# Optimization experiments

Hardware: AMD Instinct MI355X
Metric: run time of the kernel (lower is better)

## Reference

```python
import jax, jax.numpy as jnp
import numpy as np

N = 512          # pedestrians in scene
T = 12           # decode steps
OBS = 8
FEAT = 2
LAT = 32
COND = 64
LSTM_IN = 128
HID = 64         # lstm_hidden_size == context_state_size
CTX = 64
EMB = 32         # Pooling_net spatial embedding dim
MLP_IN = EMB + 2 * CTX   # 160
MLP_MID = 64
BOT = CTX        # bottleneck_dim = h_dim
IN_DEC = COND + LAT + CTX + FEAT  # 162


def setup_inputs() -> dict:
    key = jax.random.key(0)
    ks = jax.random.split(key, 24)
    s = 0.1
    return {
        "last_position": jax.random.normal(ks[0], (N, FEAT), jnp.float32),
        "c": jax.random.normal(ks[1], (N, COND), jnp.float32),
        "z": jax.random.normal(ks[2], (N, LAT), jnp.float32),
        "obs_traj_pos": jax.random.normal(ks[3], (OBS, N, FEAT), jnp.float32),
        "nei_index": jax.random.randint(ks[4], (T, N, N), 0, 2, jnp.int32),
        "nei_num_index": jax.random.randint(ks[5], (N,), 0, N, jnp.int32),
        "h0": jax.random.normal(ks[6], (N, HID), jnp.float32),
        "c0": jax.random.normal(ks[7], (N, HID), jnp.float32),
        "eps": jax.random.normal(ks[8], (T, N, FEAT), jnp.float32),
        "W_in": jax.random.normal(ks[9], (IN_DEC, LSTM_IN), jnp.float32) * s,
        "b_in": jnp.zeros((LSTM_IN,), jnp.float32),
        "W_ih": jax.random.normal(ks[10], (4 * HID, LSTM_IN), jnp.float32) * s,
        "W_hh": jax.random.normal(ks[11], (4 * HID, HID), jnp.float32) * s,
        "b_ih": jnp.zeros((4 * HID,), jnp.float32),
        "b_hh": jnp.zeros((4 * HID,), jnp.float32),
        "W_l2p": jax.random.normal(ks[12], (HID // 2 + CTX, FEAT), jnp.float32) * s,
        "b_l2p": jnp.zeros((FEAT,), jnp.float32),
        "W_sp": jax.random.normal(ks[13], (FEAT, EMB), jnp.float32) * s,
        "b_sp": jnp.zeros((EMB,), jnp.float32),
        "W1": jax.random.normal(ks[14], (MLP_IN, MLP_MID), jnp.float32) * s,
        "b1": jnp.zeros((MLP_MID,), jnp.float32),
        "W2": jax.random.normal(ks[15], (MLP_MID, BOT), jnp.float32) * s,
        "b2": jnp.zeros((BOT,), jnp.float32),
    }


def reference(last_position, c, z, obs_traj_pos, nei_index, nei_num_index,
              h0, c0, eps, W_in, b_in, W_ih, W_hh, b_ih, b_hh,
              W_l2p, b_l2p, W_sp, b_sp, W1, b1, W2, b2):
    sg = jax.lax.stop_gradient
    half = HID // 2
    neg_inf = jnp.float32(-jnp.inf)

    def pooling(mask, lstm_state, pos):
        # mask: [N,N] bool; lstm_state: [N,CTX]; pos: [N,2]
        corr = pos[:, None, :] - pos[None, :, :]           # [N,N,2] pos[i]-pos[j]
        r = corr @ W_sp + b_sp                              # [N,N,EMB]
        hj = jnp.broadcast_to(lstm_state[None, :, :], (N, N, CTX))
        hi = jnp.broadcast_to(lstm_state[:, None, :], (N, N, CTX))
        x = jnp.concatenate([r, hj, hi], axis=-1)           # [N,N,160]
        h1 = jax.nn.relu(x @ W1 + b1)
        h2 = jax.nn.relu(h1 @ W2 + b2)                      # [N,N,BOT]
        Hm = jnp.where(mask[:, :, None], h2, neg_inf)       # scatter of valid rows
        pool = Hm.max(axis=1)                               # max over neighbors j
        return jnp.where(pool == neg_inf, 0.0, pool)

    def lstm_cell(x, h, cs):
        gates = x @ W_ih.T + b_ih + h @ W_hh.T + b_hh
        i, f, g, o = jnp.split(gates, 4, axis=-1)
        c_new = jax.nn.sigmoid(f) * cs + jax.nn.sigmoid(i) * jnp.tanh(g)
        h_new = jax.nn.sigmoid(o) * jnp.tanh(c_new)
        return h_new, c_new

    def step(carry, xs):
        prev_pos, h, cs, ctx, cur_abs = carry
        nei_t, eps_t = xs
        emb = jnp.concatenate([sg(prev_pos), sg(c), sg(z), sg(ctx)], axis=-1)
        x = jax.nn.relu(emb @ W_in + b_in)
        h, cs = lstm_cell(x, h, cs)
        ctx = pooling(nei_t > 0, h, cur_abs)
        mu = jnp.concatenate([h[:, :half], ctx], -1) @ W_l2p + b_l2p
        logvar = jnp.concatenate([h[:, half:], ctx], -1) @ W_l2p + b_l2p
        pos = mu + eps_t * jnp.exp(0.5 * logvar)
        cur_abs = sg(cur_abs + pos)
        return (pos, h, cs, ctx, cur_abs), (pos, mu, logvar)

    ctx0 = jnp.zeros((N, CTX), jnp.float32)
    carry0 = (last_position, h0, c0, ctx0, obs_traj_pos[-1])
    _, (pre_pos, mean, var) = jax.lax.scan(step, carry0, (nei_index, eps))
    return pre_pos, mean, var
```

## Files before the change

### kernel.cpp

```cpp
#include <hip/hip_runtime.h>
#include <math.h>

#define NP 512
#define TT 12

typedef float f32x4 __attribute__((ext_vector_type(4)));
typedef __bf16 bf16x8 __attribute__((ext_vector_type(8)));

#define OFF_CURABS 0
#define OFF_Q      2048
#define OFF_P      67584
#define OFF_H      100352
#define OFF_CS     133120
#define OFF_XCZ    165888
#define OFF_WGB    231424
#define OFF_WCTXB  256000
#define OFF_W1B    260096
#define OFF_WIN01  264192
#define OFF_WC     264448
#define OFF_BASE   264576

__global__ __launch_bounds__(256) void init_k(
    const float* __restrict__ obs, const float* __restrict__ cc,
    const float* __restrict__ zz,
    const float* __restrict__ W_in, const float* __restrict__ W_ih,
    const float* __restrict__ W_hh, const float* __restrict__ W_sp,
    const float* __restrict__ b_sp, const float* __restrict__ W1,
    const float* __restrict__ b1, float* __restrict__ ws) {
  if (blockIdx.x < 128) {
    int id = blockIdx.x * 256 + threadIdx.x;
    if (id < 1024) ws[OFF_CURABS + id] = obs[7 * 1024 + id];
    __bf16* wgb = (__bf16*)(ws + OFF_WGB);
    for (int e = id; e < 49152; e += 32768) {
      int k = e >> 8, g = e & 255;
      float v = (k < 128) ? W_ih[g * 128 + k] : W_hh[g * 64 + (k - 128)];
      wgb[e] = (__bf16)v;
    }
    if (id < 8192) {
      int d = id >> 7, k = id & 127;
      ((__bf16*)(ws + OFF_WCTXB))[id] = (__bf16)W_in[(98 + d) * 128 + k];
    }
    if (id < 8192) {
      int r = id >> 6, m = id & 63;
      ((__bf16*)(ws + OFF_W1B))[id] = (__bf16)W1[(32 + r) * 64 + m];
    }
    if (id < 256) ws[OFF_WIN01 + id] = W_in[(id >> 7) * 128 + (id & 127)];
    if (id < 128) {
      int d = id >> 6, m = id & 63;
      float s = 0.f;
      for (int e = 0; e < 32; ++e) s = fmaf(W_sp[d * 32 + e], W1[e * 64 + m], s);
      ws[OFF_WC + id] = s;
    }
    if (id < 64) {
      float s = b1[id];
      for (int e = 0; e < 32; ++e) s = fmaf(b_sp[e], W1[e * 64 + id], s);
      ws[OFF_BASE + id] = s;
    }
  } else {
    int b = blockIdx.x - 128;
    int k = threadIdx.x;
    if (k < 128) {
      float s = 0.f;
      for (int d = 0; d < 64; ++d) s = fmaf(cc[b * 64 + d], W_in[(2 + d) * 128 + k], s);
      for (int d = 0; d < 32; ++d) s = fmaf(zz[b * 32 + d], W_in[(66 + d) * 128 + k], s);
      ws[OFF_XCZ + b * 128 + k] = s;
    }
  }
}

__global__ __launch_bounds__(256) void step_k(
    const float* __restrict__ lastpos, const int* __restrict__ nei,
    const float* __restrict__ h0, const float* __restrict__ c0,
    const float* __restrict__ obs, const float* __restrict__ epsin,
    const float* __restrict__ b_in,
    const float* __restrict__ b_ih, const float* __restrict__ b_hh,
    const float* __restrict__ Wl2p, const float* __restrict__ bl2p,
    const float* __restrict__ W2, const float* __restrict__ b2,
    float* __restrict__ out, float* __restrict__ ws, int s) {
  __shared__ __align__(16) __bf16 W2T[64 * 72];
  __shared__ int   ml[512];
  __shared__ float wcl[128], basev[64];
  __shared__ float red[4][64];
  __shared__ float hloc[64], csloc[64], ctxloc[64], prevp[2], pxy[2];
  __shared__ float xpart[2][128], xvec[128], gl[256];

  int t = threadIdx.x;
  int b = blockIdx.x;
  int lane = t & 63, w = t >> 6;
  int quad = lane >> 4, col = lane & 15;

  if (t < 64) {
    if (s == 0) { hloc[t] = h0[b * 64 + t]; csloc[t] = c0[b * 64 + t]; ctxloc[t] = 0.f; }
    else        { hloc[t] = ws[OFF_H + b * 64 + t]; csloc[t] = ws[OFF_CS + b * 64 + t]; }
    basev[t] = ws[OFF_BASE + t];
  } else if (t < 192) {
    wcl[t - 64] = ws[OFF_WC + (t - 64)];
  }
  if (s == 0 && t < 2) {
    prevp[t] = lastpos[b * 2 + t];
    pxy[t]   = obs[7 * 1024 + b * 2 + t];
  }
  if (s > 0) {
    for (int e = t; e < 4096; e += 256)
      W2T[(e & 63) * 72 + (e >> 6)] = (__bf16)W2[e];
    const int* neirow = nei + ((size_t)(s - 1) * NP + b) * NP;
    for (int j = t; j < 512; j += 256) ml[j] = neirow[j];
  }
  __syncthreads();

  if (s > 0) {
    int st = s - 1;
    const float* Qb = ws + OFF_Q + (st & 1) * 32768;
    bf16x8 bf00 = *(const bf16x8*)&W2T[(0 * 16 + col) * 72 + 0 * 32 + quad * 8];
    bf16x8 bf01 = *(const bf16x8*)&W2T[(0 * 16 + col) * 72 + 1 * 32 + quad * 8];
    bf16x8 bf10 = *(const bf16x8*)&W2T[(1 * 16 + col) * 72 + 0 * 32 + quad * 8];
    bf16x8 bf11 = *(const bf16x8*)&W2T[(1 * 16 + col) * 72 + 1 * 32 + quad * 8];
    bf16x8 bf20 = *(const bf16x8*)&W2T[(2 * 16 + col) * 72 + 0 * 32 + quad * 8];
    bf16x8 bf21 = *(const bf16x8*)&W2T[(2 * 16 + col) * 72 + 1 * 32 + quad * 8];
    bf16x8 bf30 = *(const bf16x8*)&W2T[(3 * 16 + col) * 72 + 0 * 32 + quad * 8];
    bf16x8 bf31 = *(const bf16x8*)&W2T[(3 * 16 + col) * 72 + 1 * 32 + quad * 8];
    float pl0[8], pl1[8];
    #pragma unroll
    for (int e = 0; e < 8; ++e) {
      pl0[e] = ws[OFF_P + b * 64 + quad * 8 + e];
      pl1[e] = ws[OFF_P + b * 64 + 32 + quad * 8 + e];
    }
    float vmax0 = -1e30f, vmax1 = -1e30f, vmax2 = -1e30f, vmax3 = -1e30f;

    for (int c = 0; c < 8; ++c) {
      int j0 = w * 128 + c * 16;
      int jr = (j0 + col) * 64 + quad * 8;
      f32x4 qa = *(const f32x4*)&Qb[jr];
      f32x4 qb = *(const f32x4*)&Qb[jr + 4];
      f32x4 qc = *(const f32x4*)&Qb[jr + 32];
      f32x4 qd = *(const f32x4*)&Qb[jr + 36];
      bf16x8 a0, a1;
      #pragma unroll
      for (int e = 0; e < 4; ++e) {
        a0[e]     = (__bf16)fmaxf(qa[e] + pl0[e],     0.f);
        a0[e + 4] = (__bf16)fmaxf(qb[e] + pl0[e + 4], 0.f);
        a1[e]     = (__bf16)fmaxf(qc[e] + pl1[e],     0.f);
        a1[e + 4] = (__bf16)fmaxf(qd[e] + pl1[e + 4], 0.f);
      }
      int mrow = j0 + quad * 4;
      bool mk0 = ml[mrow] > 0, mk1 = ml[mrow + 1] > 0,
           mk2 = ml[mrow + 2] > 0, mk3 = ml[mrow + 3] > 0;
      f32x4 acc;
      acc = (f32x4){0.f, 0.f, 0.f, 0.f};
      acc = __builtin_amdgcn_mfma_f32_16x16x32_bf16(a0, bf00, acc, 0, 0, 0);
      acc = __builtin_amdgcn_mfma_f32_16x16x32_bf16(a1, bf01, acc, 0, 0, 0);
      vmax0 = fmaxf(vmax0, mk0 ? acc[0] : -1e30f);
      vmax0 = fmaxf(vmax0, mk1 ? acc[1] : -1e30f);
      vmax0 = fmaxf(vmax0, mk2 ? acc[2] : -1e30f);
      vmax0 = fmaxf(vmax0, mk3 ? acc[3] : -1e30f);
      acc = (f32x4){0.f, 0.f, 0.f, 0.f};
      acc = __builtin_amdgcn_mfma_f32_16x16x32_bf16(a0, bf10, acc, 0, 0, 0);
      acc = __builtin_amdgcn_mfma_f32_16x16x32_bf16(a1, bf11, acc, 0, 0, 0);
      vmax1 = fmaxf(vmax1, mk0 ? acc[0] : -1e30f);
      vmax1 = fmaxf(vmax1, mk1 ? acc[1] : -1e30f);
      vmax1 = fmaxf(vmax1, mk2 ? acc[2] : -1e30f);
      vmax1 = fmaxf(vmax1, mk3 ? acc[3] : -1e30f);
      acc = (f32x4){0.f, 0.f, 0.f, 0.f};
      acc = __builtin_amdgcn_mfma_f32_16x16x32_bf16(a0, bf20, acc, 0, 0, 0);
      acc = __builtin_amdgcn_mfma_f32_16x16x32_bf16(a1, bf21, acc, 0, 0, 0);
      vmax2 = fmaxf(vmax2, mk0 ? acc[0] : -1e30f);
      vmax2 = fmaxf(vmax2, mk1 ? acc[1] : -1e30f);
      vmax2 = fmaxf(vmax2, mk2 ? acc[2] : -1e30f);
      vmax2 = fmaxf(vmax2, mk3 ? acc[3] : -1e30f);
      acc = (f32x4){0.f, 0.f, 0.f, 0.f};
      acc = __builtin_amdgcn_mfma_f32_16x16x32_bf16(a0, bf30, acc, 0, 0, 0);
      acc = __builtin_amdgcn_mfma_f32_16x16x32_bf16(a1, bf31, acc, 0, 0, 0);
      vmax3 = fmaxf(vmax3, mk0 ? acc[0] : -1e30f);
      vmax3 = fmaxf(vmax3, mk1 ? acc[1] : -1e30f);
      vmax3 = fmaxf(vmax3, mk2 ? acc[2] : -1e30f);
      vmax3 = fmaxf(vmax3, mk3 ? acc[3] : -1e30f);
    }
    vmax0 = fmaxf(vmax0, __shfl_xor(vmax0, 16));
    vmax0 = fmaxf(vmax0, __shfl_xor(vmax0, 32));
    vmax1 = fmaxf(vmax1, __shfl_xor(vmax1, 16));
    vmax1 = fmaxf(vmax1, __shfl_xor(vmax1, 32));
    vmax2 = fmaxf(vmax2, __shfl_xor(vmax2, 16));
    vmax2 = fmaxf(vmax2, __shfl_xor(vmax2, 32));
    vmax3 = fmaxf(vmax3, __shfl_xor(vmax3, 16));
    vmax3 = fmaxf(vmax3, __shfl_xor(vmax3, 32));
    if (lane < 16) {
      red[w][0 * 16 + lane] = vmax0;
      red[w][1 * 16 + lane] = vmax1;
      red[w][2 * 16 + lane] = vmax2;
      red[w][3 * 16 + lane] = vmax3;
    }
    __syncthreads();
    if (t < 64) {
      float m4 = fmaxf(fmaxf(red[0][t], red[1][t]),
                       fmaxf(red[2][t], red[3][t]));
      ctxloc[t] = fmaxf(m4 + b2[t], 0.f);
    }
    __syncthreads();
    if (t < 64) {
      int l = t;
      float cl = ctxloc[l];
      float sc0 = cl * Wl2p[(32 + l) * 2 + 0];
      float sc1 = cl * Wl2p[(32 + l) * 2 + 1];
      float m0 = 0.f, m1 = 0.f, v0 = 0.f, v1 = 0.f;
      if (l < 32) {
        float hm = hloc[l];
        m0 = hm * Wl2p[l * 2 + 0]; m1 = hm * Wl2p[l * 2 + 1];
        float hv = hloc[32 + l];
        v0 = hv * Wl2p[l * 2 + 0]; v1 = hv * Wl2p[l * 2 + 1];
      }
      for (int off = 32; off >= 1; off >>= 1) {
        sc0 += __shfl_down(sc0, off);
        sc1 += __shfl_down(sc1, off);
        m0  += __shfl_down(m0,  off);
        m1  += __shfl_down(m1,  off);
        v0  += __shfl_down(v0,  off);
        v1  += __shfl_down(v1,  off);
      }
      if (l == 0) {
        float mu0 = m0 + sc0 + bl2p[0], mu1 = m1 + sc1 + bl2p[1];
        float lv0 = v0 + sc0 + bl2p[0], lv1 = v1 + sc1 + bl2p[1];
        float e0 = epsin[st * 1024 + b * 2 + 0];
        float e1 = epsin[st * 1024 + b * 2 + 1];
        float p0 = mu0 + e0 * expf(0.5f * lv0);
        float p1 = mu1 + e1 * expf(0.5f * lv1);
        out[st * 1024 + b * 2 + 0] = p0;
        out[st * 1024 + b * 2 + 1] = p1;
        out[12288 + st * 1024 + b * 2 + 0] = mu0;
        out[12288 + st * 1024 + b * 2 + 1] = mu1;
        out[24576 + st * 1024 + b * 2 + 0] = lv0;
        out[24576 + st * 1024 + b * 2 + 1] = lv1;
        float px = ws[OFF_CURABS + (st & 1) * 1024 + b * 2 + 0];
        float py = ws[OFF_CURABS + (st & 1) * 1024 + b * 2 + 1];
        float nx = px + p0, ny = py + p1;
        ws[OFF_CURABS + ((st & 1) ^ 1) * 1024 + b * 2 + 0] = nx;
        ws[OFF_CURABS + ((st & 1) ^ 1) * 1024 + b * 2 + 1] = ny;
        pxy[0] = nx; pxy[1] = ny;
        prevp[0] = p0; prevp[1] = p1;
      }
    }
    __syncthreads();
  }

  if (s < TT) {
    {
      int k = t & 127, p = t >> 7;
      const __bf16* wctx = (const __bf16*)(ws + OFF_WCTXB);
      float a0 = 0.f, a1 = 0.f;
      if (p == 0)
        a0 = ws[OFF_XCZ + b * 128 + k] +
             prevp[0] * ws[OFF_WIN01 + k] + prevp[1] * ws[OFF_WIN01 + 128 + k];
      int d = p;
      for (; d + 2 < 64; d += 4) {
        a0 = fmaf(ctxloc[d],     (float)wctx[d * 128 + k],       a0);
        a1 = fmaf(ctxloc[d + 2], (float)wctx[(d + 2) * 128 + k], a1);
      }
      if (d < 64) a0 = fmaf(ctxloc[d], (float)wctx[d * 128 + k], a0);
      xpart[p][k] = a0 + a1;
    }
    __syncthreads();
    if (t < 128) xvec[t] = fmaxf(xpart[0][t] + xpart[1][t] + b_in[t], 0.f);
    __syncthreads();
    {
      int g = t;
      const __bf16* wgb = (const __bf16*)(ws + OFF_WGB);
      float s0 = 0.f, s1 = 0.f, s2 = 0.f, s3 = 0.f;
      for (int kk = 0; kk < 128; kk += 4) {
        s0 = fmaf(xvec[kk],     (float)wgb[kk * 256 + g],       s0);
        s1 = fmaf(xvec[kk + 1], (float)wgb[(kk + 1) * 256 + g], s1);
        s2 = fmaf(xvec[kk + 2], (float)wgb[(kk + 2) * 256 + g], s2);
        s3 = fmaf(xvec[kk + 3], (float)wgb[(kk + 3) * 256 + g], s3);
      }
      for (int kk = 0; kk < 64; kk += 4) {
        s0 = fmaf(hloc[kk],     (float)wgb[(128 + kk) * 256 + g],     s0);
        s1 = fmaf(hloc[kk + 1], (float)wgb[(129 + kk) * 256 + g],     s1);
        s2 = fmaf(hloc[kk + 2], (float)wgb[(130 + kk) * 256 + g],     s2);
        s3 = fmaf(hloc[kk + 3], (float)wgb[(131 + kk) * 256 + g],     s3);
      }
      gl[g] = b_ih[g] + b_hh[g] + ((s0 + s1) + (s2 + s3));
    }
    __syncthreads();
    if (t < 64) {
      float ig = gl[t], fg = gl[64 + t], gg = gl[128 + t], og = gl[192 + t];
      float is = 1.f / (1.f + expf(-ig));
      float fs = 1.f / (1.f + expf(-fg));
      float os = 1.f / (1.f + expf(-og));
      float cn = fs * csloc[t] + is * tanhf(gg);
      float hv = os * tanhf(cn);
      hloc[t] = hv;
      ws[OFF_CS + b * 64 + t] = cn;
      ws[OFF_H + b * 64 + t] = hv;
    }
    __syncthreads();
    if (t < 128) {
      int which = t >> 6, m = t & 63;
      const __bf16* wb = (const __bf16*)(ws + OFF_W1B) + which * 4096 + m;
      float s0 = 0.f, s1 = 0.f, s2 = 0.f, s3 = 0.f;
      for (int k = 0; k < 64; k += 4) {
        s0 = fmaf(hloc[k],     (float)wb[k * 64],       s0);
        s1 = fmaf(hloc[k + 1], (float)wb[(k + 1) * 64], s1);
        s2 = fmaf(hloc[k + 2], (float)wb[(k + 2) * 64], s2);
        s3 = fmaf(hloc[k + 3], (float)wb[(k + 3) * 64], s3);
      }
      float sv = (s0 + s1) + (s2 + s3);
      float cx = pxy[0], cy = pxy[1];
      if (which == 0)
        ws[OFF_Q + (s & 1) * 32768 + b * 64 + m] =
            sv + basev[m] - cx * wcl[m] - cy * wcl[64 + m];
      else
        ws[OFF_P + b * 64 + m] = sv + cx * wcl[m] + cy * wcl[64 + m];
    }
  }
}

extern "C" void kernel_launch(void* const* d_in, const int* in_sizes, int n_in,
                              void* d_out, int out_size, void* d_ws, size_t ws_size,
                              hipStream_t stream) {
  const float* lastpos = (const float*)d_in[0];
  const float* cc      = (const float*)d_in[1];
  const float* zz      = (const float*)d_in[2];
  const float* obs     = (const float*)d_in[3];
  const int*   nei     = (const int*)d_in[4];
  const float* h0      = (const float*)d_in[6];
  const float* c0      = (const float*)d_in[7];
  const float* eps     = (const float*)d_in[8];
  const float* W_in    = (const float*)d_in[9];
  const float* b_in    = (const float*)d_in[10];
  const float* W_ih    = (const float*)d_in[11];
  const float* W_hh    = (const float*)d_in[12];
  const float* b_ih    = (const float*)d_in[13];
  const float* b_hh    = (const float*)d_in[14];
  const float* W_l2p   = (const float*)d_in[15];
  const float* b_l2p   = (const float*)d_in[16];
  const float* W_sp    = (const float*)d_in[17];
  const float* b_sp    = (const float*)d_in[18];
  const float* W1      = (const float*)d_in[19];
  const float* b1      = (const float*)d_in[20];
  const float* W2      = (const float*)d_in[21];
  const float* b2      = (const float*)d_in[22];
  float* out = (float*)d_out;
  float* ws  = (float*)d_ws;

  hipLaunchKernelGGL(init_k, dim3(640), dim3(256), 0, stream,
                     obs, cc, zz, W_in, W_ih, W_hh, W_sp, b_sp, W1, b1, ws);
  for (int s = 0; s <= TT; ++s) {
    hipLaunchKernelGGL(step_k, dim3(NP), dim3(256), 0, stream,
                       lastpos, nei, h0, c0, obs, eps,
                       b_in, b_ih, b_hh, W_l2p, b_l2p,
                       W2, b2, out, ws, s);
  }
}
```

Baseline: 335.3 us.

## Store Q in bf16, pre-swizzle W2 fragments, prefetch gate weights into cache

The per-step Q buffer that every block reads in full (512x64) is now stored as bf16, which halves the dominant global read traffic in the pooling loop. W2 is pre-converted into MFMA fragment order once in the init kernel, so each block loads its fragments directly and no longer transposes W2 into shared memory every step. A dummy strided read of the gate weights is added at kernel start to warm the cache, kept alive by a never-true compare and store. Rounding Q to bf16 before the add and relu adds precision loss.

```diff
diff --git a/kernel.cpp b/kernel.cpp
--- a/kernel.cpp
+++ b/kernel.cpp
@@ -8,17 +8,18 @@
 typedef __bf16 bf16x8 __attribute__((ext_vector_type(8)));
 
 #define OFF_CURABS 0
-#define OFF_Q      2048
-#define OFF_P      67584
-#define OFF_H      100352
-#define OFF_CS     133120
-#define OFF_XCZ    165888
-#define OFF_WGB    231424
-#define OFF_WCTXB  256000
-#define OFF_W1B    260096
-#define OFF_WIN01  264192
-#define OFF_WC     264448
-#define OFF_BASE   264576
+#define OFF_QB     2048
+#define OFF_P      34816
+#define OFF_H      67584
+#define OFF_CS     100352
+#define OFF_XCZ    133120
+#define OFF_WGB    198656
+#define OFF_WCTXB  223232
+#define OFF_W1B    227328
+#define OFF_WIN01  231424
+#define OFF_WC     231680
+#define OFF_BASE   231808
+#define OFF_W2F    231872
 
 __global__ __launch_bounds__(256) void init_k(
     const float* __restrict__ obs, const float* __restrict__ cc,
@@ -26,7 +27,8 @@
     const float* __restrict__ W_in, const float* __restrict__ W_ih,
     const float* __restrict__ W_hh, const float* __restrict__ W_sp,
     const float* __restrict__ b_sp, const float* __restrict__ W1,
-    const float* __restrict__ b1, float* __restrict__ ws) {
+    const float* __restrict__ b1, const float* __restrict__ W2,
+    float* __restrict__ ws) {
   if (blockIdx.x < 128) {
     int id = blockIdx.x * 256 + threadIdx.x;
     if (id < 1024) ws[OFF_CURABS + id] = obs[7 * 1024 + id];
@@ -56,6 +58,12 @@
       for (int e = 0; e < 32; ++e) s = fmaf(b_sp[e], W1[e * 64 + id], s);
       ws[OFF_BASE + id] = s;
     }
+    if (id < 4096) {
+      int e = id & 7, f = (id >> 3) & 7, cq = id >> 6;
+      int col = cq >> 2, quad = cq & 3, mt = f >> 1, kh = f & 1;
+      ((__bf16*)(ws + OFF_W2F))[id] =
+          (__bf16)W2[(kh * 32 + quad * 8 + e) * 64 + (mt * 16 + col)];
+    }
   } else {
     int b = blockIdx.x - 128;
     int k = threadIdx.x;
@@ -75,9 +83,8 @@
     const float* __restrict__ b_in,
     const float* __restrict__ b_ih, const float* __restrict__ b_hh,
     const float* __restrict__ Wl2p, const float* __restrict__ bl2p,
-    const float* __restrict__ W2, const float* __restrict__ b2,
+    const float* __restrict__ b2,
     float* __restrict__ out, float* __restrict__ ws, int s) {
-  __shared__ __align__(16) __bf16 W2T[64 * 72];
   __shared__ int   ml[512];
   __shared__ float wcl[128], basev[64];
   __shared__ float red[4][64];
@@ -88,6 +95,13 @@
   int b = blockIdx.x;
   int lane = t & 63, w = t >> 6;
   int quad = lane >> 4, col = lane & 15;
+
+  float pf = 0.f;
+  if (s < TT) {
+    const float* wsrc = ws + OFF_WGB;
+    #pragma unroll
+    for (int k = 0; k < 4; ++k) pf += wsrc[(t + k * 256) * 24];
+  }
 
   if (t < 64) {
     if (s == 0) { hloc[t] = h0[b * 64 + t]; csloc[t] = c0[b * 64 + t]; ctxloc[t] = 0.f; }
@@ -101,24 +115,24 @@
     pxy[t]   = obs[7 * 1024 + b * 2 + t];
   }
   if (s > 0) {
-    for (int e = t; e < 4096; e += 256)
-      W2T[(e & 63) * 72 + (e >> 6)] = (__bf16)W2[e];
     const int* neirow = nei + ((size_t)(s - 1) * NP + b) * NP;
     for (int j = t; j < 512; j += 256) ml[j] = neirow[j];
   }
+  if (pf == 1.2345e-33f) ws[OFF_CURABS + 1] = pf;
   __syncthreads();
 
   if (s > 0) {
     int st = s - 1;
-    const float* Qb = ws + OFF_Q + (st & 1) * 32768;
-    bf16x8 bf00 = *(const bf16x8*)&W2T[(0 * 16 + col) * 72 + 0 * 32 + quad * 8];
-    bf16x8 bf01 = *(const bf16x8*)&W2T[(0 * 16 + col) * 72 + 1 * 32 + quad * 8];
-    bf16x8 bf10 = *(const bf16x8*)&W2T[(1 * 16 + col) * 72 + 0 * 32 + quad * 8];
-    bf16x8 bf11 = *(const bf16x8*)&W2T[(1 * 16 + col) * 72 + 1 * 32 + quad * 8];
-    bf16x8 bf20 = *(const bf16x8*)&W2T[(2 * 16 + col) * 72 + 0 * 32 + quad * 8];
-    bf16x8 bf21 = *(const bf16x8*)&W2T[(2 * 16 + col) * 72 + 1 * 32 + quad * 8];
-    bf16x8 bf30 = *(const bf16x8*)&W2T[(3 * 16 + col) * 72 + 0 * 32 + quad * 8];
-    bf16x8 bf31 = *(const bf16x8*)&W2T[(3 * 16 + col) * 72 + 1 * 32 + quad * 8];
+    const __bf16* Qb = (const __bf16*)(ws + OFF_QB) + (st & 1) * 32768;
+    const __bf16* wf = (const __bf16*)(ws + OFF_W2F) + (col * 4 + quad) * 64;
+    bf16x8 bf00 = *(const bf16x8*)&wf[0];
+    bf16x8 bf01 = *(const bf16x8*)&wf[8];
+    bf16x8 bf10 = *(const bf16x8*)&wf[16];
+    bf16x8 bf11 = *(const bf16x8*)&wf[24];
+    bf16x8 bf20 = *(const bf16x8*)&wf[32];
+    bf16x8 bf21 = *(const bf16x8*)&wf[40];
+    bf16x8 bf30 = *(const bf16x8*)&wf[48];
+    bf16x8 bf31 = *(const bf16x8*)&wf[56];
     float pl0[8], pl1[8];
     #pragma unroll
     for (int e = 0; e < 8; ++e) {
@@ -128,21 +142,16 @@
     float vmax0 = -1e30f, vmax1 = -1e30f, vmax2 = -1e30f, vmax3 = -1e30f;
 
     for (int c = 0; c < 8; ++c) {
-      int j0 = w * 128 + c * 16;
-      int jr = (j0 + col) * 64 + quad * 8;
-      f32x4 qa = *(const f32x4*)&Qb[jr];
-      f32x4 qb = *(const f32x4*)&Qb[jr + 4];
-      f32x4 qc = *(const f32x4*)&Qb[jr + 32];
-      f32x4 qd = *(const f32x4*)&Qb[jr + 36];
+      int j = w * 128 + c * 16 + col;
+      bf16x8 q0 = *(const bf16x8*)&Qb[j * 64 + quad * 8];
+      bf16x8 q1 = *(const bf16x8*)&Qb[j * 64 + 32 + quad * 8];
       bf16x8 a0, a1;
       #pragma unroll
-      for (int e = 0; e < 4; ++e) {
-        a0[e]     = (__bf16)fmaxf(qa[e] + pl0[e],     0.f);
-        a0[e + 4] = (__bf16)fmaxf(qb[e] + pl0[e + 4], 0.f);
-        a1[e]     = (__bf16)fmaxf(qc[e] + pl1[e],     0.f);
-        a1[e + 4] = (__bf16)fmaxf(qd[e] + pl1[e + 4], 0.f);
-      }
-      int mrow = j0 + quad * 4;
+      for (int e = 0; e < 8; ++e) {
+        a0[e] = (__bf16)fmaxf((float)q0[e] + pl0[e], 0.f);
+        a1[e] = (__bf16)fmaxf((float)q1[e] + pl1[e], 0.f);
+      }
+      int mrow = w * 128 + c * 16 + quad * 4;
       bool mk0 = ml[mrow] > 0, mk1 = ml[mrow + 1] > 0,
            mk2 = ml[mrow + 2] > 0, mk3 = ml[mrow + 3] > 0;
       f32x4 acc;
@@ -271,10 +280,10 @@
         s3 = fmaf(xvec[kk + 3], (float)wgb[(kk + 3) * 256 + g], s3);
       }
       for (int kk = 0; kk < 64; kk += 4) {
-        s0 = fmaf(hloc[kk],     (float)wgb[(128 + kk) * 256 + g],     s0);
-        s1 = fmaf(hloc[kk + 1], (float)wgb[(129 + kk) * 256 + g],     s1);
-        s2 = fmaf(hloc[kk + 2], (float)wgb[(130 + kk) * 256 + g],     s2);
-        s3 = fmaf(hloc[kk + 3], (float)wgb[(131 + kk) * 256 + g],     s3);
+        s0 = fmaf(hloc[kk],     (float)wgb[(128 + kk) * 256 + g], s0);
+        s1 = fmaf(hloc[kk + 1], (float)wgb[(129 + kk) * 256 + g], s1);
+        s2 = fmaf(hloc[kk + 2], (float)wgb[(130 + kk) * 256 + g], s2);
+        s3 = fmaf(hloc[kk + 3], (float)wgb[(131 + kk) * 256 + g], s3);
       }
       gl[g] = b_ih[g] + b_hh[g] + ((s0 + s1) + (s2 + s3));
     }
@@ -304,8 +313,8 @@
       float sv = (s0 + s1) + (s2 + s3);
       float cx = pxy[0], cy = pxy[1];
       if (which == 0)
-        ws[OFF_Q + (s & 1) * 32768 + b * 64 + m] =
-            sv + basev[m] - cx * wcl[m] - cy * wcl[64 + m];
+        ((__bf16*)(ws + OFF_QB))[(s & 1) * 32768 + b * 64 + m] =
+            (__bf16)(sv + basev[m] - cx * wcl[m] - cy * wcl[64 + m]);
       else
         ws[OFF_P + b * 64 + m] = sv + cx * wcl[m] + cy * wcl[64 + m];
     }
@@ -341,11 +350,11 @@
   float* ws  = (float*)d_ws;
 
   hipLaunchKernelGGL(init_k, dim3(640), dim3(256), 0, stream,
-                     obs, cc, zz, W_in, W_ih, W_hh, W_sp, b_sp, W1, b1, ws);
+                     obs, cc, zz, W_in, W_ih, W_hh, W_sp, b_sp, W1, b1, W2, ws);
   for (int s = 0; s <= TT; ++s) {
     hipLaunchKernelGGL(step_k, dim3(NP), dim3(256), 0, stream,
                        lastpos, nei, h0, c0, obs, eps,
                        b_in, b_ih, b_hh, W_l2p, b_l2p,
-                       W2, b2, out, ws, s);
+                       b2, out, ws, s);
   }
 }
```

New measurement: 336.8 us. No clear change (+0.4%).
